# Optimization experiments

Measured on AMD Instinct MI355X. Metric: run time of the kernel, lower is better.

## Reference

```python
import jax, jax.numpy as jnp
import numpy as np

N_NODES = 100000
N_EDGES = 3200000
N_FEAT = 128
EMBED = 20
N_CLASSES = 10
N_GRAPHS = 64


def setup_inputs() -> dict:
    key = jax.random.key(0)
    ks = jax.random.split(key, 8)
    x = jax.random.normal(ks[0], (N_NODES, N_FEAT), dtype=jnp.float32)
    edge_index = jax.random.randint(ks[1], (2, N_EDGES), 0, N_NODES, dtype=jnp.int64)
    edge_weights = jax.random.uniform(ks[2], (N_EDGES,), dtype=jnp.float32)
    batch = jnp.sort(jax.random.randint(ks[3], (N_NODES,), 0, N_GRAPHS, dtype=jnp.int64))
    # GCNConv parameters (glorot-ish scale) and final linear layer
    W = jax.random.normal(ks[4], (N_FEAT, EMBED), dtype=jnp.float32) * (1.0 / np.sqrt(N_FEAT))
    b = jnp.zeros((EMBED,), dtype=jnp.float32)
    lin_W = jax.random.normal(ks[5], (2 * EMBED, N_CLASSES), dtype=jnp.float32) * (1.0 / np.sqrt(2 * EMBED))
    lin_b = jnp.zeros((N_CLASSES,), dtype=jnp.float32)
    return {"x": x, "edge_index": edge_index, "edge_weights": edge_weights,
            "batch": batch, "W": W, "b": b, "lin_W": lin_W, "lin_b": lin_b}


def reference(x, edge_index, edge_weights, batch, W, b, lin_W, lin_b):
    N = x.shape[0]
    # --- GCNConv with self-loops and symmetric normalization (PyG semantics) ---
    loops = jnp.arange(N, dtype=edge_index.dtype)
    src = jnp.concatenate([edge_index[0], loops])
    dst = jnp.concatenate([edge_index[1], loops])
    w = jnp.concatenate([edge_weights, jnp.ones((N,), dtype=edge_weights.dtype)])
    deg = jax.ops.segment_sum(w, dst, num_segments=N)  # degree at targets
    dinv = jnp.where(deg > 0, jax.lax.rsqrt(deg), 0.0)
    norm = dinv[src] * w * dinv[dst]  # [E+N]
    xw = x @ W  # [N, EMBED]
    msg = xw[src] * norm[:, None]  # gather + scale
    out1 = jax.ops.segment_sum(msg, dst, num_segments=N) + b  # scatter-add
    # --- L2 normalize per node (F.normalize p=2 dim=1, eps=1e-12), then ReLU ---
    nrm = jnp.sqrt(jnp.sum(out1 * out1, axis=1, keepdims=True))
    embed = jax.nn.relu(out1 / jnp.maximum(nrm, 1e-12))
    # --- global max / mean pool per graph ---
    mx = jax.ops.segment_max(embed, batch, num_segments=N_GRAPHS)
    mx = jnp.where(jnp.isfinite(mx), mx, 0.0)  # empty graphs -> 0
    cnt = jax.ops.segment_sum(jnp.ones((N,), dtype=embed.dtype), batch, num_segments=N_GRAPHS)
    mean = jax.ops.segment_sum(embed, batch, num_segments=N_GRAPHS) / jnp.maximum(cnt, 1.0)[:, None]
    pooled = jnp.concatenate([mx, mean], axis=-1)  # [G, 2*EMBED]
    return pooled @ lin_W + lin_b
```

## Files before the change

kernel.cpp:

```cpp
#include <hip/hip_runtime.h>
#include <hip/hip_fp16.h>

#define NN 100000
#define NE 3200000
#define NF 128
#define EM 20
#define NC 10
#define NG 64

#define NB 782
#define CAPB 4608
#define T 4096
#define SBLK 512

#define ROWH 24

__global__ __launch_bounds__(SBLK) void k_scatter(
        const int* __restrict__ src, const int* __restrict__ dst,
        const float* __restrict__ w, int* __restrict__ gcursor,
        uint2* __restrict__ barr) {
    __shared__ unsigned int cnt[1024];
    __shared__ unsigned int off[1024];
    __shared__ unsigned int gbase[NB];
    __shared__ unsigned int wsum[8];
    __shared__ uint2 staged[T];
    __shared__ unsigned short bkt[T];
    int tid = threadIdx.x;
    long E0 = (long)blockIdx.x * T;
    int tot = (int)min((long)T, (long)NE - E0);
    for (int i = tid; i < 1024; i += SBLK) cnt[i] = 0;
    __syncthreads();
    unsigned int dreg[T / SBLK];
#pragma unroll
    for (int k = 0; k < T / SBLK; ++k) {
        int e = k * SBLK + tid;
        dreg[k] = 0;
        if (e < tot) {
            dreg[k] = (unsigned)dst[E0 + e];
            atomicAdd(&cnt[dreg[k] >> 7], 1u);
        }
    }
    __syncthreads();
    {
        int lane = tid & 63, wv = tid >> 6;
        unsigned int v0 = cnt[tid * 2], v1 = cnt[tid * 2 + 1];
        unsigned int ps = v0 + v1;
        unsigned int ips = ps;
#pragma unroll
        for (int o = 1; o < 64; o <<= 1) {
            unsigned int t = __shfl_up(ips, o);
            if (lane >= o) ips += t;
        }
        if (lane == 63) wsum[wv] = ips;
        __syncthreads();
        if (tid == 0) {
            unsigned int a = 0;
#pragma unroll
            for (int i = 0; i < 8; ++i) { unsigned int t = wsum[i]; wsum[i] = a; a += t; }
        }
        __syncthreads();
        unsigned int base = wsum[wv] + (ips - ps);
        off[tid * 2] = base;
        off[tid * 2 + 1] = base + v0;
    }
    __syncthreads();
    for (int i = tid; i < NB; i += SBLK) {
        unsigned int c = cnt[i];
        gbase[i] = c ? (unsigned int)atomicAdd(&gcursor[i], (int)c) : 0u;
        cnt[i] = 0;
    }
    __syncthreads();
#pragma unroll
    for (int k = 0; k < T / SBLK; ++k) {
        int e = k * SBLK + tid;
        if (e < tot) {
            long ge = E0 + e;
            unsigned int d = dreg[k];
            unsigned int b = d >> 7;
            unsigned int slot = atomicAdd(&cnt[b], 1u);
            unsigned int pos = off[b] + slot;
            staged[pos] = make_uint2((((unsigned)src[ge]) << 7) | (d & 127u),
                                     __float_as_uint(w[ge]));
            bkt[pos] = (unsigned short)b;
        }
    }
    __syncthreads();
    for (int i = tid; i < tot; i += SBLK) {
        unsigned int b = bkt[i];
        unsigned int gpos = gbase[b] + ((unsigned)i - off[b]);
        if (gpos < CAPB) barr[(size_t)b * CAPB + gpos] = staged[i];
    }
}

__global__ __launch_bounds__(1024) void k_sortb(const int* __restrict__ gcursor,
                                                unsigned long long* __restrict__ barr64,
                                                int* __restrict__ rowptrs,
                                                float* __restrict__ dinv) {
    __shared__ unsigned long long srt[CAPB];
    __shared__ unsigned int cnt[128];
    __shared__ unsigned int off[128];
    int bk = blockIdx.x, tid = threadIdx.x;
    if (tid < 128) cnt[tid] = 0;
    __syncthreads();
    int cntb = min(gcursor[bk], CAPB);
    unsigned long long* row = barr64 + (size_t)bk * CAPB;
    unsigned long long rec[5];
    unsigned int pos[5];
    int K = 0;
    for (int e = tid; e < cntb; e += 1024) {
        rec[K] = row[e];
        pos[K] = atomicAdd(&cnt[(unsigned)rec[K] & 127u], 1u);
        ++K;
    }
    __syncthreads();
    if (tid < 128) off[tid] = cnt[tid];
    __syncthreads();
    for (int d = 1; d < 128; d <<= 1) {
        unsigned int v = 0;
        if (tid < 128 && tid >= (unsigned)d) v = off[tid - d];
        __syncthreads();
        if (tid < 128 && tid >= (unsigned)d) off[tid] += v;
        __syncthreads();
    }
    for (int k = 0; k < K; ++k) {
        unsigned int dl = (unsigned)rec[k] & 127u;
        srt[off[dl] - cnt[dl] + pos[k]] = rec[k];
    }
    __syncthreads();
    for (int e = tid; e < cntb; e += 1024) row[e] = srt[e];
    if (tid < 128) rowptrs[bk * 129 + tid] = (int)(off[tid] - cnt[tid]);
    if (tid == 0) rowptrs[bk * 129 + 128] = cntb;
    if (tid < 128) {
        unsigned int s0 = off[tid] - cnt[tid], s1 = off[tid];
        float s = 1.0f;
        for (unsigned int i = s0; i < s1; ++i)
            s += __uint_as_float((unsigned int)(srt[i] >> 32));
        int gd = bk * 128 + tid;
        if (gd < NN) dinv[gd] = rsqrtf(s);
    }
}

__global__ void k_xw(const float* __restrict__ x, const float* __restrict__ W,
                     const float* __restrict__ dinv, __half* __restrict__ xwh) {
    __shared__ float xs[64 * 129];
    __shared__ float Ws[NF * EM];
    int base = blockIdx.x * 64;
    for (int i = threadIdx.x; i < NF * EM; i += 256) Ws[i] = W[i];
    const float4* xg = (const float4*)(x + (size_t)base * NF);
    for (int v = threadIdx.x; v < 64 * NF / 4; v += 256) {
        int fidx = v * 4;
        size_t gidx = (size_t)base * NF + fidx;
        float4 val = (gidx + 3 < (size_t)NN * NF) ? xg[v] : make_float4(0.f, 0.f, 0.f, 0.f);
        int r = fidx / NF, c = fidx % NF;
        float* p = xs + r * 129 + c;
        p[0] = val.x; p[1] = val.y; p[2] = val.z; p[3] = val.w;
    }
    __syncthreads();
    int n = threadIdx.x & 63;
    int jg = threadIdx.x >> 6;
    int j0 = jg * 5;
    if (base + n >= NN) return;
    float acc[5] = {0.f, 0.f, 0.f, 0.f, 0.f};
    const float* xr = xs + n * 129;
#pragma unroll 4
    for (int k = 0; k < NF; ++k) {
        float xv = xr[k];
        const float* wr = Ws + k * EM + j0;
#pragma unroll
        for (int jj = 0; jj < 5; ++jj) acc[jj] = fmaf(xv, wr[jj], acc[jj]);
    }
    float dv = dinv[base + n];
    __half* ph = xwh + (size_t)(base + n) * ROWH + j0;
#pragma unroll
    for (int jj = 0; jj < 5; ++jj) ph[jj] = __float2half(acc[jj] * dv);
}

__device__ inline void unpack20(uint4 a, uint4 bq, uint2 cq, float* f) {
    const __half2* h = (const __half2*)&a;
#pragma unroll
    for (int c = 0; c < 4; ++c) { float2 t = __half22float2(h[c]); f[2*c] = t.x; f[2*c+1] = t.y; }
    h = (const __half2*)&bq;
#pragma unroll
    for (int c = 0; c < 4; ++c) { float2 t = __half22float2(h[c]); f[8+2*c] = t.x; f[9+2*c] = t.y; }
    h = (const __half2*)&cq;
#pragma unroll
    for (int c = 0; c < 2; ++c) { float2 t = __half22float2(h[c]); f[16+2*c] = t.x; f[17+2*c] = t.y; }
}

__global__ __launch_bounds__(512) void k_aggr(
        const int* __restrict__ rowptrs, const unsigned long long* __restrict__ barr64,
        const __half* __restrict__ xwh, const float* __restrict__ dinv,
        const float* __restrict__ b, float* __restrict__ embed) {
    int bk = blockIdx.x, tid = threadIdx.x;
    int d = tid >> 2, sub = tid & 3;
    int s0 = rowptrs[bk * 129 + d], s1 = rowptrs[bk * 129 + d + 1];
    const unsigned long long* row = barr64 + (size_t)bk * CAPB;
    const uint4* plane = (const uint4*)xwh;
    float acc[20];
#pragma unroll
    for (int j = 0; j < 20; ++j) acc[j] = 0.f;
    for (int e = s0 + sub; e < s1; e += 4) {
        unsigned long long r = row[e];
        unsigned int s = ((unsigned int)r) >> 7;
        float nw = __uint_as_float((unsigned int)(r >> 32));
        const uint4* p4 = plane + (size_t)s * 3;
        uint4 a = p4[0];
        uint4 bq = p4[1];
        uint2 cq = *(const uint2*)(p4 + 2);
        float f[20];
        unpack20(a, bq, cq, f);
#pragma unroll
        for (int j = 0; j < 20; ++j) acc[j] = fmaf(f[j], nw, acc[j]);
    }
#pragma unroll
    for (int j = 0; j < 20; ++j) {
        acc[j] += __shfl_xor(acc[j], 1);
        acc[j] += __shfl_xor(acc[j], 2);
    }
    if (sub == 0) {
        int gd = bk * 128 + d;
        if (gd < NN) {
            float dv = dinv[gd];
            const uint4* p4 = plane + (size_t)gd * 3;
            uint4 a = p4[0];
            uint4 bq = p4[1];
            uint2 cq = *(const uint2*)(p4 + 2);
            float xdh[20];
            unpack20(a, bq, cq, xdh);
            float r[20];
            float ss = 0.f;
#pragma unroll
            for (int j = 0; j < 20; ++j) {
                r[j] = dv * (acc[j] + xdh[j]) + b[j];
                ss = fmaf(r[j], r[j], ss);
            }
            float inv = 1.0f / fmaxf(sqrtf(ss), 1e-12f);
            float4 o4[5];
            float* o = (float*)o4;
#pragma unroll
            for (int j = 0; j < 20; ++j) {
                float e = r[j] * inv;
                o[j] = e > 0.f ? e : 0.f;
            }
            float4* eo = (float4*)(embed + (size_t)gd * EM);
#pragma unroll
            for (int c = 0; c < 5; ++c) eo[c] = o4[c];
        }
    }
}

__global__ void k_bound(const int* __restrict__ batch, int* __restrict__ gstart) {
    int n = blockIdx.x * 256 + threadIdx.x;
    if (n >= NN) return;
    int bn = batch[n];
    if (n == 0) {
        for (int g = 0; g <= bn; ++g) gstart[g] = 0;
    } else {
        int bp = batch[n - 1];
        for (int g = bp + 1; g <= bn; ++g) gstart[g] = n;
    }
    if (n == NN - 1) {
        for (int g = bn + 1; g <= NG; ++g) gstart[g] = NN;
    }
}

__global__ void k_poolfinal(const float* __restrict__ embed, const int* __restrict__ gstart,
                            const float* __restrict__ lw, const float* __restrict__ lb,
                            float* __restrict__ out) {
    __shared__ float cross[4][40];
    __shared__ float pooled[40];
    int g = blockIdx.x;
    int s0 = gstart[g], s1 = gstart[g + 1];
    int cnt = s1 - s0;
    float mx[EM], sm[EM];
#pragma unroll
    for (int j = 0; j < EM; ++j) { mx[j] = 0.f; sm[j] = 0.f; }
    for (int n = s0 + threadIdx.x; n < s1; n += 256) {
        const float4* e = (const float4*)(embed + (size_t)n * EM);
#pragma unroll
        for (int c = 0; c < 5; ++c) {
            float4 v = e[c];
            int j = c * 4;
            mx[j+0] = fmaxf(mx[j+0], v.x); sm[j+0] += v.x;
            mx[j+1] = fmaxf(mx[j+1], v.y); sm[j+1] += v.y;
            mx[j+2] = fmaxf(mx[j+2], v.z); sm[j+2] += v.z;
            mx[j+3] = fmaxf(mx[j+3], v.w); sm[j+3] += v.w;
        }
    }
#pragma unroll
    for (int o = 32; o > 0; o >>= 1) {
#pragma unroll
        for (int j = 0; j < EM; ++j) {
            mx[j] = fmaxf(mx[j], __shfl_xor(mx[j], o));
            sm[j] += __shfl_xor(sm[j], o);
        }
    }
    int wave = threadIdx.x >> 6, lane = threadIdx.x & 63;
    if (lane == 0) {
#pragma unroll
        for (int j = 0; j < EM; ++j) { cross[wave][j] = mx[j]; cross[wave][EM + j] = sm[j]; }
    }
    __syncthreads();
    if (threadIdx.x < 40) {
        int j = threadIdx.x;
        float v = cross[0][j];
        if (j < EM) v = fmaxf(fmaxf(v, cross[1][j]), fmaxf(cross[2][j], cross[3][j]));
        else        v = v + cross[1][j] + cross[2][j] + cross[3][j];
        if (j >= EM) v *= 1.0f / fmaxf((float)cnt, 1.0f);
        pooled[j] = v;
    }
    __syncthreads();
    if (threadIdx.x < NC) {
        int c = threadIdx.x;
        float acc = lb[c];
#pragma unroll
        for (int j = 0; j < 2 * EM; ++j) acc = fmaf(pooled[j], lw[j * NC + c], acc);
        out[g * NC + c] = acc;
    }
}

static inline size_t align_up(size_t v) { return (v + 1023) & ~(size_t)1023; }

extern "C" void kernel_launch(void* const* d_in, const int* in_sizes, int n_in,
                              void* d_out, int out_size, void* d_ws, size_t ws_size,
                              hipStream_t stream) {
    const float* x     = (const float*)d_in[0];
    const int*   ei    = (const int*)d_in[1];
    const float* ew    = (const float*)d_in[2];
    const int*   batch = (const int*)d_in[3];
    const float* W     = (const float*)d_in[4];
    const float* b     = (const float*)d_in[5];
    const float* lw    = (const float*)d_in[6];
    const float* lb    = (const float*)d_in[7];
    float* out = (float*)d_out;

    char* ws = (char*)d_ws;
    int*    gcursor = (int*)ws;    ws += align_up(4096);
    int*    gstart  = (int*)ws;    ws += align_up(1024);
    int*    rowptrs = (int*)ws;    ws += align_up((size_t)NB * 129 * 4);
    float*  dinv    = (float*)ws;  ws += align_up((size_t)NN * 4);
    __half* xwh     = (__half*)ws; ws += align_up((size_t)NN * ROWH * 2);
    float*  embed   = (float*)ws;  ws += align_up((size_t)NN * EM * 4);
    uint2*  barr    = (uint2*)ws;
    unsigned long long* barr64 = (unsigned long long*)barr;

    const int* srcp = ei;
    const int* dstp = ei + NE;

    (void)hipMemsetAsync(gcursor, 0, 4096, stream);
    k_scatter<<<(NE + T - 1) / T, SBLK, 0, stream>>>(srcp, dstp, ew, gcursor, barr);
    k_sortb<<<NB, 1024, 0, stream>>>(gcursor, barr64, rowptrs, dinv);
    k_xw<<<(NN + 63) / 64, 256, 0, stream>>>(x, W, dinv, xwh);
    k_aggr<<<NB, 512, 0, stream>>>(rowptrs, barr64, xwh, dinv, b, embed);
    k_bound<<<(NN + 255) / 256, 256, 0, stream>>>(batch, gstart);
    k_poolfinal<<<NG, 256, 0, stream>>>(embed, gstart, lw, lb, out);
}
```

Before: 266.3 us.

## Fuse bucket sort into aggregation, split degree pass, and drop boundary kernel

The per-bucket sort is moved into the aggregation kernel, which sorts the bucket in shared memory and reads edges from there. This avoids writing the sorted edges and row pointers back to global memory and reading them again. Degree computation becomes a separate light kernel that uses shared-memory float atomics. Other changes: the scatter block grows to 1024 threads, the half-precision xw rows are split into a 16-wide and a 4-wide plane for aligned loads, and the graph-boundary kernel is replaced by binary search inside pooling. The edge records are now read twice (degree kernel and aggregation), and atomic float summation makes degree results nondeterministic in rounding order.

```diff
diff --git a/kernel.cpp b/kernel.cpp
--- a/kernel.cpp
+++ b/kernel.cpp
@@ -11,9 +11,7 @@
 #define NB 782
 #define CAPB 4608
 #define T 4096
-#define SBLK 512
-
-#define ROWH 24
+#define SBLK 1024
 
 __global__ __launch_bounds__(SBLK) void k_scatter(
         const int* __restrict__ src, const int* __restrict__ dst,
@@ -22,13 +20,13 @@
     __shared__ unsigned int cnt[1024];
     __shared__ unsigned int off[1024];
     __shared__ unsigned int gbase[NB];
-    __shared__ unsigned int wsum[8];
+    __shared__ unsigned int wsum[16];
     __shared__ uint2 staged[T];
     __shared__ unsigned short bkt[T];
     int tid = threadIdx.x;
     long E0 = (long)blockIdx.x * T;
     int tot = (int)min((long)T, (long)NE - E0);
-    for (int i = tid; i < 1024; i += SBLK) cnt[i] = 0;
+    cnt[tid] = 0;
     __syncthreads();
     unsigned int dreg[T / SBLK];
 #pragma unroll
@@ -43,31 +41,28 @@
     __syncthreads();
     {
         int lane = tid & 63, wv = tid >> 6;
-        unsigned int v0 = cnt[tid * 2], v1 = cnt[tid * 2 + 1];
-        unsigned int ps = v0 + v1;
-        unsigned int ips = ps;
+        unsigned int v = cnt[tid];
+        unsigned int s = v;
 #pragma unroll
         for (int o = 1; o < 64; o <<= 1) {
-            unsigned int t = __shfl_up(ips, o);
-            if (lane >= o) ips += t;
-        }
-        if (lane == 63) wsum[wv] = ips;
+            unsigned int t = __shfl_up(s, o);
+            if (lane >= o) s += t;
+        }
+        if (lane == 63) wsum[wv] = s;
         __syncthreads();
         if (tid == 0) {
             unsigned int a = 0;
 #pragma unroll
-            for (int i = 0; i < 8; ++i) { unsigned int t = wsum[i]; wsum[i] = a; a += t; }
+            for (int i = 0; i < 16; ++i) { unsigned int t = wsum[i]; wsum[i] = a; a += t; }
         }
         __syncthreads();
-        unsigned int base = wsum[wv] + (ips - ps);
-        off[tid * 2] = base;
-        off[tid * 2 + 1] = base + v0;
-    }
-    __syncthreads();
-    for (int i = tid; i < NB; i += SBLK) {
-        unsigned int c = cnt[i];
-        gbase[i] = c ? (unsigned int)atomicAdd(&gcursor[i], (int)c) : 0u;
-        cnt[i] = 0;
+        off[tid] = wsum[wv] + s - v;
+    }
+    __syncthreads();
+    if (tid < NB) {
+        unsigned int c = cnt[tid];
+        gbase[tid] = c ? (unsigned int)atomicAdd(&gcursor[tid], (int)c) : 0u;
+        cnt[tid] = 0;
     }
     __syncthreads();
 #pragma unroll
@@ -92,56 +87,28 @@
     }
 }
 
-__global__ __launch_bounds__(1024) void k_sortb(const int* __restrict__ gcursor,
-                                                unsigned long long* __restrict__ barr64,
-                                                int* __restrict__ rowptrs,
-                                                float* __restrict__ dinv) {
-    __shared__ unsigned long long srt[CAPB];
-    __shared__ unsigned int cnt[128];
-    __shared__ unsigned int off[128];
+__global__ void k_degb(const int* __restrict__ gcursor, const uint2* __restrict__ barr,
+                       float* __restrict__ dinv) {
+    __shared__ float dacc[128];
     int bk = blockIdx.x, tid = threadIdx.x;
-    if (tid < 128) cnt[tid] = 0;
+    if (tid < 128) dacc[tid] = 0.f;
     __syncthreads();
     int cntb = min(gcursor[bk], CAPB);
-    unsigned long long* row = barr64 + (size_t)bk * CAPB;
-    unsigned long long rec[5];
-    unsigned int pos[5];
-    int K = 0;
-    for (int e = tid; e < cntb; e += 1024) {
-        rec[K] = row[e];
-        pos[K] = atomicAdd(&cnt[(unsigned)rec[K] & 127u], 1u);
-        ++K;
-    }
-    __syncthreads();
-    if (tid < 128) off[tid] = cnt[tid];
-    __syncthreads();
-    for (int d = 1; d < 128; d <<= 1) {
-        unsigned int v = 0;
-        if (tid < 128 && tid >= (unsigned)d) v = off[tid - d];
-        __syncthreads();
-        if (tid < 128 && tid >= (unsigned)d) off[tid] += v;
-        __syncthreads();
-    }
-    for (int k = 0; k < K; ++k) {
-        unsigned int dl = (unsigned)rec[k] & 127u;
-        srt[off[dl] - cnt[dl] + pos[k]] = rec[k];
-    }
-    __syncthreads();
-    for (int e = tid; e < cntb; e += 1024) row[e] = srt[e];
-    if (tid < 128) rowptrs[bk * 129 + tid] = (int)(off[tid] - cnt[tid]);
-    if (tid == 0) rowptrs[bk * 129 + 128] = cntb;
+    const uint2* row = barr + (size_t)bk * CAPB;
+    for (int i = tid; i < cntb; i += 1024) {
+        uint2 r = row[i];
+        atomicAdd(&dacc[r.x & 127u], __uint_as_float(r.y));
+    }
+    __syncthreads();
     if (tid < 128) {
-        unsigned int s0 = off[tid] - cnt[tid], s1 = off[tid];
-        float s = 1.0f;
-        for (unsigned int i = s0; i < s1; ++i)
-            s += __uint_as_float((unsigned int)(srt[i] >> 32));
         int gd = bk * 128 + tid;
-        if (gd < NN) dinv[gd] = rsqrtf(s);
+        if (gd < NN) dinv[gd] = rsqrtf(1.0f + dacc[tid]);
     }
 }
 
 __global__ void k_xw(const float* __restrict__ x, const float* __restrict__ W,
-                     const float* __restrict__ dinv, __half* __restrict__ xwh) {
+                     const float* __restrict__ dinv,
+                     __half* __restrict__ xwhA, __half* __restrict__ xwhB) {
     __shared__ float xs[64 * 129];
     __shared__ float Ws[NF * EM];
     int base = blockIdx.x * 64;
@@ -170,45 +137,90 @@
         for (int jj = 0; jj < 5; ++jj) acc[jj] = fmaf(xv, wr[jj], acc[jj]);
     }
     float dv = dinv[base + n];
-    __half* ph = xwh + (size_t)(base + n) * ROWH + j0;
-#pragma unroll
-    for (int jj = 0; jj < 5; ++jj) ph[jj] = __float2half(acc[jj] * dv);
-}
-
-__device__ inline void unpack20(uint4 a, uint4 bq, uint2 cq, float* f) {
-    const __half2* h = (const __half2*)&a;
+#pragma unroll
+    for (int jj = 0; jj < 5; ++jj) {
+        int j = j0 + jj;
+        __half hv = __float2half(acc[jj] * dv);
+        if (j < 16) xwhA[(size_t)(base + n) * 16 + j] = hv;
+        else        xwhB[(size_t)(base + n) * 4 + (j - 16)] = hv;
+    }
+}
+
+__device__ inline void unpack16(uint4 a0, uint4 a1, float* f) {
+    const __half2* h = (const __half2*)&a0;
 #pragma unroll
     for (int c = 0; c < 4; ++c) { float2 t = __half22float2(h[c]); f[2*c] = t.x; f[2*c+1] = t.y; }
-    h = (const __half2*)&bq;
+    h = (const __half2*)&a1;
 #pragma unroll
     for (int c = 0; c < 4; ++c) { float2 t = __half22float2(h[c]); f[8+2*c] = t.x; f[9+2*c] = t.y; }
-    h = (const __half2*)&cq;
-#pragma unroll
-    for (int c = 0; c < 2; ++c) { float2 t = __half22float2(h[c]); f[16+2*c] = t.x; f[17+2*c] = t.y; }
-}
-
-__global__ __launch_bounds__(512) void k_aggr(
-        const int* __restrict__ rowptrs, const unsigned long long* __restrict__ barr64,
-        const __half* __restrict__ xwh, const float* __restrict__ dinv,
-        const float* __restrict__ b, float* __restrict__ embed) {
+}
+__device__ inline void unpack4(uint2 b0, float* f) {
+    const __half2* h = (const __half2*)&b0;
+#pragma unroll
+    for (int c = 0; c < 2; ++c) { float2 t = __half22float2(h[c]); f[2*c] = t.x; f[2*c+1] = t.y; }
+}
+
+__global__ void k_sortaggr(const int* __restrict__ gcursor,
+                           const unsigned long long* __restrict__ barr64,
+                           const __half* __restrict__ xwhA, const __half* __restrict__ xwhB,
+                           const float* __restrict__ dinv, const float* __restrict__ b,
+                           float* __restrict__ embed) {
+    __shared__ unsigned long long srt[CAPB];
+    __shared__ unsigned int cnt[128];
+    __shared__ unsigned int off[128];
+    __shared__ unsigned int wtot;
     int bk = blockIdx.x, tid = threadIdx.x;
+    if (tid < 128) cnt[tid] = 0;
+    __syncthreads();
+    int cntb = min(gcursor[bk], CAPB);
+    const unsigned long long* row = barr64 + (size_t)bk * CAPB;
+    unsigned long long rec[9];
+    unsigned int pos[9];
+    int K = 0;
+    for (int e = tid; e < cntb; e += 512) {
+        rec[K] = row[e];
+        pos[K] = atomicAdd(&cnt[(unsigned)rec[K] & 127u], 1u);
+        ++K;
+    }
+    __syncthreads();
+    unsigned int v = 0, s = 0;
+    if (tid < 128) {
+        v = cnt[tid]; s = v;
+#pragma unroll
+        for (int o = 1; o < 64; o <<= 1) {
+            unsigned int t = __shfl_up(s, o);
+            if ((tid & 63) >= o) s += t;
+        }
+        if (tid == 63) wtot = s;
+    }
+    __syncthreads();
+    if (tid < 128) {
+        if (tid >= 64) s += wtot;
+        off[tid] = s;
+    }
+    __syncthreads();
+    for (int k = 0; k < K; ++k) {
+        unsigned int dl = (unsigned)rec[k] & 127u;
+        srt[off[dl] - cnt[dl] + pos[k]] = rec[k];
+    }
+    __syncthreads();
     int d = tid >> 2, sub = tid & 3;
-    int s0 = rowptrs[bk * 129 + d], s1 = rowptrs[bk * 129 + d + 1];
-    const unsigned long long* row = barr64 + (size_t)bk * CAPB;
-    const uint4* plane = (const uint4*)xwh;
+    int s0 = (int)(off[d] - cnt[d]), s1 = (int)off[d];
+    const uint4* pA = (const uint4*)xwhA;
+    const uint2* pB = (const uint2*)xwhB;
     float acc[20];
 #pragma unroll
     for (int j = 0; j < 20; ++j) acc[j] = 0.f;
     for (int e = s0 + sub; e < s1; e += 4) {
-        unsigned long long r = row[e];
-        unsigned int s = ((unsigned int)r) >> 7;
+        unsigned long long r = srt[e];
+        unsigned int sN = ((unsigned int)r) >> 7;
         float nw = __uint_as_float((unsigned int)(r >> 32));
-        const uint4* p4 = plane + (size_t)s * 3;
-        uint4 a = p4[0];
-        uint4 bq = p4[1];
-        uint2 cq = *(const uint2*)(p4 + 2);
+        uint4 a0 = pA[(size_t)sN * 2];
+        uint4 a1 = pA[(size_t)sN * 2 + 1];
+        uint2 b0 = pB[sN];
         float f[20];
-        unpack20(a, bq, cq, f);
+        unpack16(a0, a1, f);
+        unpack4(b0, f + 16);
 #pragma unroll
         for (int j = 0; j < 20; ++j) acc[j] = fmaf(f[j], nw, acc[j]);
     }
@@ -221,12 +233,12 @@
         int gd = bk * 128 + d;
         if (gd < NN) {
             float dv = dinv[gd];
-            const uint4* p4 = plane + (size_t)gd * 3;
-            uint4 a = p4[0];
-            uint4 bq = p4[1];
-            uint2 cq = *(const uint2*)(p4 + 2);
+            uint4 a0 = pA[(size_t)gd * 2];
+            uint4 a1 = pA[(size_t)gd * 2 + 1];
+            uint2 b0 = pB[gd];
             float xdh[20];
-            unpack20(a, bq, cq, xdh);
+            unpack16(a0, a1, xdh);
+            unpack4(b0, xdh + 16);
             float r[20];
             float ss = 0.f;
 #pragma unroll
@@ -239,8 +251,8 @@
             float* o = (float*)o4;
 #pragma unroll
             for (int j = 0; j < 20; ++j) {
-                float e = r[j] * inv;
-                o[j] = e > 0.f ? e : 0.f;
+                float e2 = r[j] * inv;
+                o[j] = e2 > 0.f ? e2 : 0.f;
             }
             float4* eo = (float4*)(embed + (size_t)gd * EM);
 #pragma unroll
@@ -249,28 +261,22 @@
     }
 }
 
-__global__ void k_bound(const int* __restrict__ batch, int* __restrict__ gstart) {
-    int n = blockIdx.x * 256 + threadIdx.x;
-    if (n >= NN) return;
-    int bn = batch[n];
-    if (n == 0) {
-        for (int g = 0; g <= bn; ++g) gstart[g] = 0;
-    } else {
-        int bp = batch[n - 1];
-        for (int g = bp + 1; g <= bn; ++g) gstart[g] = n;
-    }
-    if (n == NN - 1) {
-        for (int g = bn + 1; g <= NG; ++g) gstart[g] = NN;
-    }
-}
-
-__global__ void k_poolfinal(const float* __restrict__ embed, const int* __restrict__ gstart,
+__device__ inline int lbound(const int* __restrict__ batch, int key) {
+    int lo = 0, hi = NN;
+    while (lo < hi) {
+        int mid = (lo + hi) >> 1;
+        if (batch[mid] < key) lo = mid + 1; else hi = mid;
+    }
+    return lo;
+}
+
+__global__ void k_poolfinal(const float* __restrict__ embed, const int* __restrict__ batch,
                             const float* __restrict__ lw, const float* __restrict__ lb,
                             float* __restrict__ out) {
     __shared__ float cross[4][40];
     __shared__ float pooled[40];
     int g = blockIdx.x;
-    int s0 = gstart[g], s1 = gstart[g + 1];
+    int s0 = lbound(batch, g), s1 = lbound(batch, g + 1);
     int cnt = s1 - s0;
     float mx[EM], sm[EM];
 #pragma unroll
@@ -336,10 +342,9 @@
 
     char* ws = (char*)d_ws;
     int*    gcursor = (int*)ws;    ws += align_up(4096);
-    int*    gstart  = (int*)ws;    ws += align_up(1024);
-    int*    rowptrs = (int*)ws;    ws += align_up((size_t)NB * 129 * 4);
     float*  dinv    = (float*)ws;  ws += align_up((size_t)NN * 4);
-    __half* xwh     = (__half*)ws; ws += align_up((size_t)NN * ROWH * 2);
+    __half* xwhA    = (__half*)ws; ws += align_up((size_t)NN * 16 * 2);
+    __half* xwhB    = (__half*)ws; ws += align_up((size_t)NN * 4 * 2);
     float*  embed   = (float*)ws;  ws += align_up((size_t)NN * EM * 4);
     uint2*  barr    = (uint2*)ws;
     unsigned long long* barr64 = (unsigned long long*)barr;
@@ -349,9 +354,8 @@
 
     (void)hipMemsetAsync(gcursor, 0, 4096, stream);
     k_scatter<<<(NE + T - 1) / T, SBLK, 0, stream>>>(srcp, dstp, ew, gcursor, barr);
-    k_sortb<<<NB, 1024, 0, stream>>>(gcursor, barr64, rowptrs, dinv);
-    k_xw<<<(NN + 63) / 64, 256, 0, stream>>>(x, W, dinv, xwh);
-    k_aggr<<<NB, 512, 0, stream>>>(rowptrs, barr64, xwh, dinv, b, embed);
-    k_bound<<<(NN + 255) / 256, 256, 0, stream>>>(batch, gstart);
-    k_poolfinal<<<NG, 256, 0, stream>>>(embed, gstart, lw, lb, out);
-}
+    k_degb<<<NB, 1024, 0, stream>>>(gcursor, barr, dinv);
+    k_xw<<<(NN + 63) / 64, 256, 0, stream>>>(x, W, dinv, xwhA, xwhB);
+    k_sortaggr<<<NB, 512, 0, stream>>>(gcursor, barr64, xwhA, xwhB, dinv, b, embed);
+    k_poolfinal<<<NG, 256, 0, stream>>>(embed, batch, lw, lb, out);
+}
```

New measurement: 266.0 us, median of 2. Within noise of the previous version (-0.1%).
